# Performance work log

Measured on AMD Instinct MI355X. Metric: run time of the kernel, lower is better.

## Reference

```python
import jax, jax.numpy as jnp
import numpy as np
from jax.ops import segment_sum

N = 100000
E = 1600000
IN_DIM = 128
HID_DIM = 128
OUT_DIM = 64
BN_EPS = 1e-5


def setup_inputs() -> dict:
    key = jax.random.key(0)
    ks = jax.random.split(key, 8)
    h = jax.random.normal(ks[0], (N, IN_DIM), dtype=jnp.float32)
    src = jax.random.randint(ks[1], (E,), 0, N, dtype=jnp.int32)
    dst = jax.random.randint(ks[2], (E,), 0, N, dtype=jnp.int32)
    # GraphConv weights (glorot-ish scale)
    W1 = jax.random.normal(ks[3], (IN_DIM, HID_DIM), dtype=jnp.float32) / np.sqrt(IN_DIM)
    b1 = jnp.zeros((HID_DIM,), dtype=jnp.float32)
    W2 = jax.random.normal(ks[4], (HID_DIM, OUT_DIM), dtype=jnp.float32) / np.sqrt(HID_DIM)
    b2 = jnp.zeros((OUT_DIM,), dtype=jnp.float32)
    gamma = jnp.ones((HID_DIM,), dtype=jnp.float32)
    beta = jnp.zeros((HID_DIM,), dtype=jnp.float32)
    return {"h": h, "W1": W1, "b1": b1, "W2": W2, "b2": b2,
            "gamma": gamma, "beta": beta, "src": src, "dst": dst}


def _graph_conv(h, W, b, src, dst):
    # DGL GraphConv, norm='both':
    # out = D_dst^{-1/2} * A^T (D_src^{-1/2} * h) W + b, degrees clamped to >=1
    ones = jnp.ones((E,), dtype=h.dtype)
    deg_out = jnp.clip(segment_sum(ones, src, num_segments=N), 1.0)  # out-degree of src
    deg_in = jnp.clip(segment_sum(ones, dst, num_segments=N), 1.0)   # in-degree of dst
    h = h * jax.lax.rsqrt(deg_out)[:, None]
    # apply weight before aggregation when it reduces/keeps dim (DGL optimization)
    if W.shape[0] >= W.shape[1]:
        h = h @ W
        agg = segment_sum(h[src], dst, num_segments=N)  # [N, out_feat]
    else:
        agg = segment_sum(h[src], dst, num_segments=N) @ W
    return agg * jax.lax.rsqrt(deg_in)[:, None] + b


def reference(h, W1, b1, W2, b2, gamma, beta, src, dst):
    h = _graph_conv(h, W1, b1, src, dst)           # [N, HID_DIM]
    # BatchNorm1d, training mode: batch stats over node axis, biased variance
    mean = jnp.mean(h, axis=0)
    var = jnp.mean((h - mean) ** 2, axis=0)
    h = (h - mean) * jax.lax.rsqrt(var + BN_EPS) * gamma + beta
    h = jax.nn.relu(h)
    # dropout p=0.0 -> identity
    h = _graph_conv(h, W2, b2, src, dst)           # [N, OUT_DIM]
    return h
```

## Files before the change

### kernel.cpp

```cpp
#include <hip/hip_runtime.h>

#define NN 100000
#define NE 1600000
#define NB 391
#define CAP 5120
#define EPB 4096
#define BN_EPS 1e-5f

typedef _Float16 f16;
typedef _Float16 f16x4 __attribute__((ext_vector_type(4)));
typedef _Float16 f16x8 __attribute__((ext_vector_type(8)));
typedef float f32x4v __attribute__((ext_vector_type(4)));

__global__ __launch_bounds__(256) void kInit(const float* __restrict__ W1,
                                             const float* __restrict__ W2,
                                             f16* __restrict__ W1t,
                                             f16* __restrict__ W2t,
                                             int* __restrict__ curD,
                                             int* __restrict__ curS,
                                             float* __restrict__ stats) {
    int idx = blockIdx.x * 256 + threadIdx.x;
    if (idx < NB) { curD[idx] = idx * CAP; curS[idx] = idx * CAP; }
    if (idx < 512) stats[idx] = 0.f;
    if (idx < 16384) {
        int n = idx >> 7, k = idx & 127;
        W1t[idx] = (f16)W1[k * 128 + n];
    } else if (idx < 24576) {
        int j = idx - 16384;
        int n = j >> 7, k = j & 127;
        W2t[j] = (f16)W2[k * 64 + n];
    }
}

__global__ __launch_bounds__(256) void kC(const int* __restrict__ src,
                                          const int* __restrict__ dst,
                                          int* __restrict__ curD,
                                          int* __restrict__ curS,
                                          unsigned* __restrict__ pairs,
                                          unsigned char* __restrict__ srcBuck) {
    __shared__ int hD[NB], hS[NB], bD_[NB], bS_[NB];
    for (int i = threadIdx.x; i < NB; i += 256) { hD[i] = 0; hS[i] = 0; }
    __syncthreads();
    int e0 = blockIdx.x * EPB;
    int e1 = min(e0 + EPB, NE);
    for (int e = e0 + threadIdx.x; e < e1; e += 256) {
        atomicAdd(&hD[dst[e] >> 8], 1);
        atomicAdd(&hS[src[e] >> 8], 1);
    }
    __syncthreads();
    for (int i = threadIdx.x; i < NB; i += 256) {
        bD_[i] = hD[i] ? atomicAdd(&curD[i], hD[i]) : 0;
        bS_[i] = hS[i] ? atomicAdd(&curS[i], hS[i]) : 0;
        hD[i] = 0; hS[i] = 0;
    }
    __syncthreads();
    for (int e = e0 + threadIdx.x; e < e1; e += 256) {
        int d = dst[e], s = src[e];
        int db = d >> 8, sb = s >> 8;
        int rD = atomicAdd(&hD[db], 1);
        int posD = bD_[db] + rD;
        int limD = (db + 1) * CAP - 1;
        if (posD > limD) posD = limD;
        pairs[posD] = ((unsigned)s << 8) | (unsigned)(d & 255);
        int rS = atomicAdd(&hS[sb], 1);
        int posS = bS_[sb] + rS;
        int limS = (sb + 1) * CAP - 1;
        if (posS > limS) posS = limS;
        srcBuck[posS] = (unsigned char)(s & 255);
    }
}

__global__ __launch_bounds__(256) void kDE(const unsigned* __restrict__ pairs,
                                           const unsigned char* __restrict__ srcBuck,
                                           const int* __restrict__ curD,
                                           const int* __restrict__ curS,
                                           int* __restrict__ rowS,
                                           int* __restrict__ rowE,
                                           int* __restrict__ col,
                                           int* __restrict__ degO) {
    __shared__ int cnt[256], s[256];
    int t = threadIdx.x;
    if (blockIdx.x < NB) {
        int b = blockIdx.x;
        int p0 = b * CAP, p1 = curD[b];
        cnt[t] = 0;
        __syncthreads();
        for (int p = p0 + t; p < p1; p += 256)
            atomicAdd(&cnt[pairs[p] & 255u], 1);
        __syncthreads();
        int v = cnt[t];
        s[t] = v;
        __syncthreads();
        for (int off = 1; off < 256; off <<= 1) {
            int x = (t >= off) ? s[t - off] : 0;
            __syncthreads();
            s[t] += x;
            __syncthreads();
        }
        int excl = s[t] - v;
        int node = b * 256 + t;
        if (node < NN) { rowS[node] = p0 + excl; rowE[node] = p0 + excl + v; }
        cnt[t] = excl;
        __syncthreads();
        for (int p = p0 + t; p < p1; p += 256) {
            unsigned e = pairs[p];
            int r = atomicAdd(&cnt[e & 255u], 1);
            col[p0 + r] = (int)(e >> 8);
        }
    } else {
        int b = blockIdx.x - NB;
        int p0 = b * CAP, p1 = curS[b];
        cnt[t] = 0;
        __syncthreads();
        for (int p = p0 + t; p < p1; p += 256)
            atomicAdd(&cnt[srcBuck[p]], 1);
        __syncthreads();
        int node = b * 256 + t;
        if (node < NN) degO[node] = cnt[t];
    }
}

__global__ __launch_bounds__(256) void k_gemm1(const float* __restrict__ h,
                                               const f16* __restrict__ W1t,
                                               const int* __restrict__ degO,
                                               f16* __restrict__ x1h) {
    __shared__ f16 Ah[128 * 128];
    __shared__ f16 Bt[128 * 128];
    int tid = threadIdx.x;
    int row0 = blockIdx.x * 128;
#pragma unroll
    for (int p = 0; p < 8; ++p) {
        int fi = p * 256 + tid;
        int r = fi >> 4, c = fi & 15;
        uint4 v = *(const uint4*)&W1t[fi * 8];
        *(uint4*)&Bt[r * 128 + ((c ^ (r & 7)) * 8)] = v;
    }
#pragma unroll
    for (int p = 0; p < 16; ++p) {
        int fi = p * 256 + tid;
        int r = fi >> 5, c4 = fi & 31;
        int grow = row0 + r;
        float4 av = float4{0.f, 0.f, 0.f, 0.f};
        float dv = 1.f;
        if (grow < NN) {
            av = *(const float4*)&h[(size_t)grow * 128 + c4 * 4];
            dv = (float)degO[grow];
        }
        float rs = rsqrtf(fmaxf(dv, 1.f));
        f16x4 t;
        t[0] = (f16)(av.x * rs); t[1] = (f16)(av.y * rs);
        t[2] = (f16)(av.z * rs); t[3] = (f16)(av.w * rs);
        int c8 = c4 >> 1, off = (c4 & 1) * 4;
        *(f16x4*)&Ah[r * 128 + ((c8 ^ (r & 7)) * 8) + off] = t;
    }
    __syncthreads();
    int l = tid & 63, w = tid >> 6;
    int lr = l & 15, g = l >> 4;
    int m0 = w * 32;
    f16x8 a[2][4];
#pragma unroll
    for (int m = 0; m < 2; ++m)
#pragma unroll
        for (int kk = 0; kk < 4; ++kk) {
            int row = m0 + m * 16 + lr;
            a[m][kk] = *(f16x8*)&Ah[row * 128 + (((kk * 4 + g) ^ (row & 7)) * 8)];
        }
    f32x4v acc[2][8];
#pragma unroll
    for (int m = 0; m < 2; ++m)
#pragma unroll
        for (int n = 0; n < 8; ++n) acc[m][n] = f32x4v{0.f, 0.f, 0.f, 0.f};
#pragma unroll
    for (int n = 0; n < 8; ++n) {
        int colr = n * 16 + lr;
        f16x8 b[4];
#pragma unroll
        for (int kk = 0; kk < 4; ++kk)
            b[kk] = *(f16x8*)&Bt[colr * 128 + (((kk * 4 + g) ^ (colr & 7)) * 8)];
#pragma unroll
        for (int m = 0; m < 2; ++m)
#pragma unroll
            for (int kk = 0; kk < 4; ++kk)
                acc[m][n] = __builtin_amdgcn_mfma_f32_16x16x32_f16(a[m][kk], b[kk], acc[m][n], 0, 0, 0);
    }
    __syncthreads();
#pragma unroll
    for (int m = 0; m < 2; ++m)
#pragma unroll
        for (int n = 0; n < 8; ++n)
#pragma unroll
            for (int q = 0; q < 4; ++q) {
                int row = m0 + m * 16 + g * 4 + q;
                Ah[row * 128 + n * 16 + lr] = (f16)acc[m][n][q];
            }
    __syncthreads();
#pragma unroll
    for (int p = 0; p < 8; ++p) {
        int idx = p * 64 + l;
        int r = idx >> 4, c = idx & 15;
        int row = m0 + r, grow = row0 + row;
        uint4 v = *(uint4*)&Ah[row * 128 + c * 8];
        if (grow < NN) *(uint4*)&x1h[(size_t)grow * 128 + c * 8] = v;
    }
}

__global__ __launch_bounds__(256) void k_gather1(const f16* __restrict__ x1h,
                                                 const int* __restrict__ rowS,
                                                 const int* __restrict__ rowE,
                                                 const int* __restrict__ col,
                                                 const float* __restrict__ b1,
                                                 f16* __restrict__ y1h) {
    int node = blockIdx.x * 16 + (threadIdx.x >> 4);
    int f8 = threadIdx.x & 15;
    if (node >= NN) return;
    int s0 = rowS[node], s1 = rowE[node];
    const uint4* x4 = (const uint4*)x1h;
    float acc[8] = {0.f, 0.f, 0.f, 0.f, 0.f, 0.f, 0.f, 0.f};
    int j = s0;
    for (; j + 7 < s1; j += 8) {
        uint4 v[8];
#pragma unroll
        for (int u = 0; u < 8; ++u)
            v[u] = x4[(size_t)col[j + u] * 16 + f8];
#pragma unroll
        for (int u = 0; u < 8; ++u) {
            const f16* hp = (const f16*)&v[u];
#pragma unroll
            for (int k = 0; k < 8; ++k) acc[k] += (float)hp[k];
        }
    }
    for (; j + 3 < s1; j += 4) {
        uint4 v[4];
#pragma unroll
        for (int u = 0; u < 4; ++u)
            v[u] = x4[(size_t)col[j + u] * 16 + f8];
#pragma unroll
        for (int u = 0; u < 4; ++u) {
            const f16* hp = (const f16*)&v[u];
#pragma unroll
            for (int k = 0; k < 8; ++k) acc[k] += (float)hp[k];
        }
    }
    for (; j < s1; ++j) {
        uint4 v = x4[(size_t)col[j] * 16 + f8];
        const f16* hp = (const f16*)&v;
#pragma unroll
        for (int k = 0; k < 8; ++k) acc[k] += (float)hp[k];
    }
    float rs = rsqrtf(fmaxf((float)(s1 - s0), 1.f));
    const float4* b4 = (const float4*)b1;
    float4 ba = b4[f8 * 2], bb = b4[f8 * 2 + 1];
    f16x8 o;
    o[0] = (f16)(acc[0] * rs + ba.x); o[1] = (f16)(acc[1] * rs + ba.y);
    o[2] = (f16)(acc[2] * rs + ba.z); o[3] = (f16)(acc[3] * rs + ba.w);
    o[4] = (f16)(acc[4] * rs + bb.x); o[5] = (f16)(acc[5] * rs + bb.y);
    o[6] = (f16)(acc[6] * rs + bb.z); o[7] = (f16)(acc[7] * rs + bb.w);
    *(f16x8*)&y1h[(size_t)node * 128 + f8 * 8] = o;
}

__global__ __launch_bounds__(256) void k_bnstats(const f16* __restrict__ y1h,
                                                 float* __restrict__ stats) {
    int f = threadIdx.x & 127;
    int ro = threadIdx.x >> 7;
    float s = 0.f, ss = 0.f;
    for (int i = blockIdx.x * 2 + ro; i < NN; i += gridDim.x * 2) {
        float v = (float)y1h[(size_t)i * 128 + f];
        s += v;
        ss += v * v;
    }
    atomicAdd(&stats[f], s);
    atomicAdd(&stats[128 + f], ss);
}

__global__ __launch_bounds__(128) void k_bnfinal(float* __restrict__ stats,
                                                 const float* __restrict__ gamma,
                                                 const float* __restrict__ beta) {
    int f = threadIdx.x;
    float mean = stats[f] * (1.f / NN);
    float var = stats[128 + f] * (1.f / NN) - mean * mean;
    var = fmaxf(var, 0.f);
    float sc = gamma[f] * rsqrtf(var + BN_EPS);
    stats[256 + f] = sc;
    stats[384 + f] = beta[f] - mean * sc;
}

__global__ __launch_bounds__(256) void k_gemm2(const f16* __restrict__ y1h,
                                               const f16* __restrict__ W2t,
                                               const int* __restrict__ degO,
                                               const float* __restrict__ stats,
                                               f16* __restrict__ x2h) {
    __shared__ f16 Ah[128 * 128];
    __shared__ f16 Bt[64 * 128];
    __shared__ float sc[128], sh[128];
    int tid = threadIdx.x;
    int row0 = blockIdx.x * 128;
    if (tid < 128) { sc[tid] = stats[256 + tid]; sh[tid] = stats[384 + tid]; }
#pragma unroll
    for (int p = 0; p < 4; ++p) {
        int fi = p * 256 + tid;
        int r = fi >> 4, c = fi & 15;
        uint4 v = *(const uint4*)&W2t[fi * 8];
        *(uint4*)&Bt[r * 128 + ((c ^ (r & 7)) * 8)] = v;
    }
    __syncthreads();
#pragma unroll
    for (int p = 0; p < 8; ++p) {
        int fi = p * 256 + tid;
        int r = fi >> 4, c = fi & 15;
        int grow = row0 + r;
        f16x8 t;
        if (grow < NN) {
            uint4 v = *(const uint4*)&y1h[(size_t)grow * 128 + c * 8];
            const f16* hp = (const f16*)&v;
            float rs = rsqrtf(fmaxf((float)degO[grow], 1.f));
#pragma unroll
            for (int i = 0; i < 8; ++i) {
                int ch = c * 8 + i;
                float x = (float)hp[i] * sc[ch] + sh[ch];
                t[i] = (f16)(fmaxf(x, 0.f) * rs);
            }
        } else {
#pragma unroll
            for (int i = 0; i < 8; ++i) t[i] = (f16)0.f;
        }
        *(f16x8*)&Ah[r * 128 + ((c ^ (r & 7)) * 8)] = t;
    }
    __syncthreads();
    int l = tid & 63, w = tid >> 6;
    int lr = l & 15, g = l >> 4;
    int m0 = w * 32;
    f16x8 a[2][4];
#pragma unroll
    for (int m = 0; m < 2; ++m)
#pragma unroll
        for (int kk = 0; kk < 4; ++kk) {
            int row = m0 + m * 16 + lr;
            a[m][kk] = *(f16x8*)&Ah[row * 128 + (((kk * 4 + g) ^ (row & 7)) * 8)];
        }
    f32x4v acc[2][4];
#pragma unroll
    for (int m = 0; m < 2; ++m)
#pragma unroll
        for (int n = 0; n < 4; ++n) acc[m][n] = f32x4v{0.f, 0.f, 0.f, 0.f};
#pragma unroll
    for (int n = 0; n < 4; ++n) {
        int colr = n * 16 + lr;
        f16x8 b[4];
#pragma unroll
        for (int kk = 0; kk < 4; ++kk)
            b[kk] = *(f16x8*)&Bt[colr * 128 + (((kk * 4 + g) ^ (colr & 7)) * 8)];
#pragma unroll
        for (int m = 0; m < 2; ++m)
#pragma unroll
            for (int kk = 0; kk < 4; ++kk)
                acc[m][n] = __builtin_amdgcn_mfma_f32_16x16x32_f16(a[m][kk], b[kk], acc[m][n], 0, 0, 0);
    }
    __syncthreads();
#pragma unroll
    for (int m = 0; m < 2; ++m)
#pragma unroll
        for (int n = 0; n < 4; ++n)
#pragma unroll
            for (int q = 0; q < 4; ++q) {
                int row = m0 + m * 16 + g * 4 + q;
                Ah[row * 64 + n * 16 + lr] = (f16)acc[m][n][q];
            }
    __syncthreads();
#pragma unroll
    for (int p = 0; p < 4; ++p) {
        int idx = p * 64 + l;
        int r = idx >> 3, c = idx & 7;
        int row = m0 + r, grow = row0 + row;
        uint4 v = *(uint4*)&Ah[row * 64 + c * 8];
        if (grow < NN) *(uint4*)&x2h[(size_t)grow * 64 + c * 8] = v;
    }
}

__global__ __launch_bounds__(256) void k_gather2(const f16* __restrict__ x2h,
                                                 const int* __restrict__ rowS,
                                                 const int* __restrict__ rowE,
                                                 const int* __restrict__ col,
                                                 const float* __restrict__ b2,
                                                 float* __restrict__ out) {
    int node = blockIdx.x * 32 + (threadIdx.x >> 3);
    int f8 = threadIdx.x & 7;
    if (node >= NN) return;
    int s0 = rowS[node], s1 = rowE[node];
    const uint4* x4 = (const uint4*)x2h;
    float acc[8] = {0.f, 0.f, 0.f, 0.f, 0.f, 0.f, 0.f, 0.f};
    int j = s0;
    for (; j + 7 < s1; j += 8) {
        uint4 v[8];
#pragma unroll
        for (int u = 0; u < 8; ++u)
            v[u] = x4[(size_t)col[j + u] * 8 + f8];
#pragma unroll
        for (int u = 0; u < 8; ++u) {
            const f16* hp = (const f16*)&v[u];
#pragma unroll
            for (int k = 0; k < 8; ++k) acc[k] += (float)hp[k];
        }
    }
    for (; j + 3 < s1; j += 4) {
        uint4 v[4];
#pragma unroll
        for (int u = 0; u < 4; ++u)
            v[u] = x4[(size_t)col[j + u] * 8 + f8];
#pragma unroll
        for (int u = 0; u < 4; ++u) {
            const f16* hp = (const f16*)&v[u];
#pragma unroll
            for (int k = 0; k < 8; ++k) acc[k] += (float)hp[k];
        }
    }
    for (; j < s1; ++j) {
        uint4 v = x4[(size_t)col[j] * 8 + f8];
        const f16* hp = (const f16*)&v;
#pragma unroll
        for (int k = 0; k < 8; ++k) acc[k] += (float)hp[k];
    }
    float rs = rsqrtf(fmaxf((float)(s1 - s0), 1.f));
    const float4* b4 = (const float4*)b2;
    float4 ba = b4[f8 * 2], bb = b4[f8 * 2 + 1];
    float4 o0, o1;
    o0.x = acc[0] * rs + ba.x; o0.y = acc[1] * rs + ba.y;
    o0.z = acc[2] * rs + ba.z; o0.w = acc[3] * rs + ba.w;
    o1.x = acc[4] * rs + bb.x; o1.y = acc[5] * rs + bb.y;
    o1.z = acc[6] * rs + bb.z; o1.w = acc[7] * rs + bb.w;
    *(float4*)&out[(size_t)node * 64 + f8 * 8] = o0;
    *(float4*)&out[(size_t)node * 64 + f8 * 8 + 4] = o1;
}

extern "C" void kernel_launch(void* const* d_in, const int* in_sizes, int n_in,
                              void* d_out, int out_size, void* d_ws, size_t ws_size,
                              hipStream_t stream) {
    const float* h     = (const float*)d_in[0];
    const float* W1    = (const float*)d_in[1];
    const float* b1    = (const float*)d_in[2];
    const float* W2    = (const float*)d_in[3];
    const float* b2    = (const float*)d_in[4];
    const float* gamma = (const float*)d_in[5];
    const float* beta  = (const float*)d_in[6];
    const int*   src   = (const int*)d_in[7];
    const int*   dst   = (const int*)d_in[8];
    float* out = (float*)d_out;

    const size_t BSZ = (size_t)NB * CAP;

    int* base = (int*)d_ws;
    float* stats = (float*)base;
    int* curD = base + 512;
    int* curS = curD + NB;
    int* rowS = curS + NB;
    int* rowE = rowS + NN;
    int* degO = rowE + NN;
    int* col  = degO + NN;
    unsigned* pairs = (unsigned*)(col + BSZ);
    unsigned char* srcBuck = (unsigned char*)(pairs + BSZ);
    size_t o = (size_t)(col + BSZ - base) + BSZ + (BSZ + 3) / 4;
    o = (o + 3) & ~(size_t)3;
    f16* W1t = (f16*)(base + o);
    f16* W2t = W1t + 16384;
    o += 8192 + 4096;
    f16* x1h = (f16*)(base + o);
    o += (size_t)NN * 64;
    f16* y1h = (f16*)(base + o);
    f16* x2h = x1h;

    kInit<<<97, 256, 0, stream>>>(W1, W2, W1t, W2t, curD, curS, stats);

    int bgrid = (NE + EPB - 1) / EPB;
    kC<<<bgrid, 256, 0, stream>>>(src, dst, curD, curS, pairs, srcBuck);
    kDE<<<2 * NB, 256, 0, stream>>>(pairs, srcBuck, curD, curS, rowS, rowE, col, degO);

    int ggrid = (NN + 127) / 128;
    k_gemm1<<<ggrid, 256, 0, stream>>>(h, W1t, degO, x1h);
    k_gather1<<<(NN + 15) / 16, 256, 0, stream>>>(x1h, rowS, rowE, col, b1, y1h);
    k_bnstats<<<512, 256, 0, stream>>>(y1h, stats);
    k_bnfinal<<<1, 128, 0, stream>>>(stats, gamma, beta);
    k_gemm2<<<ggrid, 256, 0, stream>>>(y1h, W2t, degO, stats, x2h);
    k_gather2<<<(NN + 31) / 32, 256, 0, stream>>>(x2h, rowS, rowE, col, b2, out);
}
```

Baseline: 275.4 us.

## Fuse BN stats into gather1, stage edges in LDS, two-pass CSR sort

Several changes at once. BatchNorm sum and sum-of-squares are now computed inside the first gather kernel via wave shuffles and per-block partials, followed by a small reduction kernel. This removes the separate pass that re-read y1h. The edge-bucketing kernel caches src/dst in shared memory instead of reading them twice. The CSR build stages each bucket in LDS and does a coarse radix pass before the per-node scatter, which should make writes to col more local. The GEMMs compute the degree normalisation once per row in shared memory. The gather loops drop the 8-way unrolled path, which may reduce memory-level parallelism.

```diff
diff --git a/kernel.cpp b/kernel.cpp
--- a/kernel.cpp
+++ b/kernel.cpp
@@ -5,6 +5,7 @@
 #define NB 391
 #define CAP 5120
 #define EPB 4096
+#define NG1 6250
 #define BN_EPS 1e-5f
 
 typedef _Float16 f16;
@@ -38,24 +39,28 @@
                                           int* __restrict__ curS,
                                           unsigned* __restrict__ pairs,
                                           unsigned char* __restrict__ srcBuck) {
+    __shared__ int sA[EPB], dA[EPB];
     __shared__ int hD[NB], hS[NB], bD_[NB], bS_[NB];
-    for (int i = threadIdx.x; i < NB; i += 256) { hD[i] = 0; hS[i] = 0; }
+    int t = threadIdx.x;
+    for (int i = t; i < NB; i += 256) { hD[i] = 0; hS[i] = 0; }
     __syncthreads();
     int e0 = blockIdx.x * EPB;
-    int e1 = min(e0 + EPB, NE);
-    for (int e = e0 + threadIdx.x; e < e1; e += 256) {
-        atomicAdd(&hD[dst[e] >> 8], 1);
-        atomicAdd(&hS[src[e] >> 8], 1);
-    }
-    __syncthreads();
-    for (int i = threadIdx.x; i < NB; i += 256) {
+    int ne = min(EPB, NE - e0);
+    for (int i = t; i < ne; i += 256) {
+        int s = src[e0 + i], d = dst[e0 + i];
+        sA[i] = s; dA[i] = d;
+        atomicAdd(&hD[d >> 8], 1);
+        atomicAdd(&hS[s >> 8], 1);
+    }
+    __syncthreads();
+    for (int i = t; i < NB; i += 256) {
         bD_[i] = hD[i] ? atomicAdd(&curD[i], hD[i]) : 0;
         bS_[i] = hS[i] ? atomicAdd(&curS[i], hS[i]) : 0;
         hD[i] = 0; hS[i] = 0;
     }
     __syncthreads();
-    for (int e = e0 + threadIdx.x; e < e1; e += 256) {
-        int d = dst[e], s = src[e];
+    for (int i = t; i < ne; i += 256) {
+        int s = sA[i], d = dA[i];
         int db = d >> 8, sb = s >> 8;
         int rD = atomicAdd(&hD[db], 1);
         int posD = bD_[db] + rD;
@@ -78,40 +83,56 @@
                                            int* __restrict__ rowE,
                                            int* __restrict__ col,
                                            int* __restrict__ degO) {
-    __shared__ int cnt[256], s[256];
+    __shared__ unsigned bufA[CAP], bufB[CAP];
+    __shared__ int binC[256], binS[256];
+    __shared__ int cnt[256], csc[256];
     int t = threadIdx.x;
     if (blockIdx.x < NB) {
         int b = blockIdx.x;
-        int p0 = b * CAP, p1 = curD[b];
-        cnt[t] = 0;
-        __syncthreads();
-        for (int p = p0 + t; p < p1; p += 256)
-            atomicAdd(&cnt[pairs[p] & 255u], 1);
-        __syncthreads();
-        int v = cnt[t];
-        s[t] = v;
+        int p0 = b * CAP;
+        int n = min(curD[b] - p0, CAP);
+        binC[t] = 0; cnt[t] = 0;
+        __syncthreads();
+        for (int i = t; i < n; i += 256) {
+            unsigned v = pairs[p0 + i];
+            bufA[i] = v;
+            atomicAdd(&binC[v >> 17], 1);
+            atomicAdd(&cnt[v & 255u], 1);
+        }
+        __syncthreads();
+        int vB = binC[t], vN = cnt[t];
+        binS[t] = vB; csc[t] = vN;
         __syncthreads();
         for (int off = 1; off < 256; off <<= 1) {
-            int x = (t >= off) ? s[t - off] : 0;
+            int xB = (t >= off) ? binS[t - off] : 0;
+            int xN = (t >= off) ? csc[t - off] : 0;
             __syncthreads();
-            s[t] += x;
+            binS[t] += xB; csc[t] += xN;
             __syncthreads();
         }
-        int excl = s[t] - v;
         int node = b * 256 + t;
-        if (node < NN) { rowS[node] = p0 + excl; rowE[node] = p0 + excl + v; }
-        cnt[t] = excl;
-        __syncthreads();
-        for (int p = p0 + t; p < p1; p += 256) {
-            unsigned e = pairs[p];
-            int r = atomicAdd(&cnt[e & 255u], 1);
-            col[p0 + r] = (int)(e >> 8);
+        int nodeStart = csc[t] - vN;
+        if (node < NN) { rowS[node] = p0 + nodeStart; rowE[node] = p0 + nodeStart + vN; }
+        binC[t] = binS[t] - vB;
+        cnt[t] = nodeStart;
+        __syncthreads();
+        for (int i = t; i < n; i += 256) {
+            unsigned v = bufA[i];
+            int pos = atomicAdd(&binC[v >> 17], 1);
+            bufB[pos] = v;
+        }
+        __syncthreads();
+        for (int i = t; i < n; i += 256) {
+            unsigned v = bufB[i];
+            int r = atomicAdd(&cnt[v & 255u], 1);
+            col[p0 + r] = (int)(v >> 8);
         }
     } else {
         int b = blockIdx.x - NB;
-        int p0 = b * CAP, p1 = curS[b];
         cnt[t] = 0;
         __syncthreads();
+        int p0 = b * CAP;
+        int p1 = min(curS[b], p0 + CAP);
         for (int p = p0 + t; p < p1; p += 256)
             atomicAdd(&cnt[srcBuck[p]], 1);
         __syncthreads();
@@ -126,8 +147,14 @@
                                                f16* __restrict__ x1h) {
     __shared__ f16 Ah[128 * 128];
     __shared__ f16 Bt[128 * 128];
+    __shared__ float rsA[128];
     int tid = threadIdx.x;
     int row0 = blockIdx.x * 128;
+    if (tid < 128) {
+        int r = row0 + tid;
+        float d = (r < NN) ? (float)degO[r] : 1.f;
+        rsA[tid] = rsqrtf(fmaxf(d, 1.f));
+    }
 #pragma unroll
     for (int p = 0; p < 8; ++p) {
         int fi = p * 256 + tid;
@@ -135,18 +162,15 @@
         uint4 v = *(const uint4*)&W1t[fi * 8];
         *(uint4*)&Bt[r * 128 + ((c ^ (r & 7)) * 8)] = v;
     }
+    __syncthreads();
 #pragma unroll
     for (int p = 0; p < 16; ++p) {
         int fi = p * 256 + tid;
         int r = fi >> 5, c4 = fi & 31;
         int grow = row0 + r;
         float4 av = float4{0.f, 0.f, 0.f, 0.f};
-        float dv = 1.f;
-        if (grow < NN) {
-            av = *(const float4*)&h[(size_t)grow * 128 + c4 * 4];
-            dv = (float)degO[grow];
-        }
-        float rs = rsqrtf(fmaxf(dv, 1.f));
+        if (grow < NN) av = *(const float4*)&h[(size_t)grow * 128 + c4 * 4];
+        float rs = rsA[r];
         f16x4 t;
         t[0] = (f16)(av.x * rs); t[1] = (f16)(av.y * rs);
         t[2] = (f16)(av.z * rs); t[3] = (f16)(av.w * rs);
@@ -209,40 +233,32 @@
                                                  const int* __restrict__ rowE,
                                                  const int* __restrict__ col,
                                                  const float* __restrict__ b1,
-                                                 f16* __restrict__ y1h) {
-    int node = blockIdx.x * 16 + (threadIdx.x >> 4);
-    int f8 = threadIdx.x & 15;
-    if (node >= NN) return;
+                                                 f16* __restrict__ y1h,
+                                                 float* __restrict__ part) {
+    __shared__ float red[4 * 16 * 16];
+    int tid = threadIdx.x;
+    int bid = blockIdx.x;
+    int node = bid * 16 + (tid >> 4);
+    int f8 = tid & 15;
     int s0 = rowS[node], s1 = rowE[node];
     const uint4* x4 = (const uint4*)x1h;
     float acc[8] = {0.f, 0.f, 0.f, 0.f, 0.f, 0.f, 0.f, 0.f};
     int j = s0;
-    for (; j + 7 < s1; j += 8) {
-        uint4 v[8];
-#pragma unroll
-        for (int u = 0; u < 8; ++u)
-            v[u] = x4[(size_t)col[j + u] * 16 + f8];
-#pragma unroll
-        for (int u = 0; u < 8; ++u) {
-            const f16* hp = (const f16*)&v[u];
-#pragma unroll
-            for (int k = 0; k < 8; ++k) acc[k] += (float)hp[k];
-        }
-    }
     for (; j + 3 < s1; j += 4) {
-        uint4 v[4];
-#pragma unroll
-        for (int u = 0; u < 4; ++u)
-            v[u] = x4[(size_t)col[j + u] * 16 + f8];
-#pragma unroll
-        for (int u = 0; u < 4; ++u) {
-            const f16* hp = (const f16*)&v[u];
-#pragma unroll
-            for (int k = 0; k < 8; ++k) acc[k] += (float)hp[k];
-        }
+        int a0 = col[j], a1 = col[j + 1], a2 = col[j + 2], a3 = col[j + 3];
+        uint4 v0 = x4[(size_t)a0 * 16 + f8];
+        uint4 v1 = x4[(size_t)a1 * 16 + f8];
+        uint4 v2 = x4[(size_t)a2 * 16 + f8];
+        uint4 v3 = x4[(size_t)a3 * 16 + f8];
+        const f16* h0 = (const f16*)&v0; const f16* h1 = (const f16*)&v1;
+        const f16* h2 = (const f16*)&v2; const f16* h3 = (const f16*)&v3;
+#pragma unroll
+        for (int k = 0; k < 8; ++k)
+            acc[k] += (float)h0[k] + (float)h1[k] + (float)h2[k] + (float)h3[k];
     }
     for (; j < s1; ++j) {
-        uint4 v = x4[(size_t)col[j] * 16 + f8];
+        int a = col[j];
+        uint4 v = x4[(size_t)a * 16 + f8];
         const f16* hp = (const f16*)&v;
 #pragma unroll
         for (int k = 0; k < 8; ++k) acc[k] += (float)hp[k];
@@ -256,20 +272,40 @@
     o[4] = (f16)(acc[4] * rs + bb.x); o[5] = (f16)(acc[5] * rs + bb.y);
     o[6] = (f16)(acc[6] * rs + bb.z); o[7] = (f16)(acc[7] * rs + bb.w);
     *(f16x8*)&y1h[(size_t)node * 128 + f8 * 8] = o;
-}
-
-__global__ __launch_bounds__(256) void k_bnstats(const f16* __restrict__ y1h,
-                                                 float* __restrict__ stats) {
-    int f = threadIdx.x & 127;
-    int ro = threadIdx.x >> 7;
-    float s = 0.f, ss = 0.f;
-    for (int i = blockIdx.x * 2 + ro; i < NN; i += gridDim.x * 2) {
-        float v = (float)y1h[(size_t)i * 128 + f];
-        s += v;
-        ss += v * v;
-    }
-    atomicAdd(&stats[f], s);
-    atomicAdd(&stats[128 + f], ss);
+    float sv[8], qv[8];
+#pragma unroll
+    for (int k = 0; k < 8; ++k) { sv[k] = (float)o[k]; qv[k] = sv[k] * sv[k]; }
+#pragma unroll
+    for (int mask = 16; mask <= 32; mask <<= 1) {
+#pragma unroll
+        for (int k = 0; k < 8; ++k) {
+            sv[k] += __shfl_xor(sv[k], mask);
+            qv[k] += __shfl_xor(qv[k], mask);
+        }
+    }
+    int w = tid >> 6, lane = tid & 63;
+    if (lane < 16) {
+#pragma unroll
+        for (int k = 0; k < 8; ++k) {
+            red[w * 256 + lane * 16 + k] = sv[k];
+            red[w * 256 + lane * 16 + 8 + k] = qv[k];
+        }
+    }
+    __syncthreads();
+    int f8_ = tid & 15, idx = tid >> 4;
+    float tot = red[0 * 256 + f8_ * 16 + idx] + red[1 * 256 + f8_ * 16 + idx]
+              + red[2 * 256 + f8_ * 16 + idx] + red[3 * 256 + f8_ * 16 + idx];
+    int slot = (idx < 8) ? (f8_ * 8 + idx) : (128 + f8_ * 8 + (idx - 8));
+    part[(size_t)bid * 256 + slot] = tot;
+}
+
+__global__ __launch_bounds__(256) void k_bnred(const float* __restrict__ part,
+                                               float* __restrict__ stats) {
+    int t = threadIdx.x;
+    float loc = 0.f;
+    for (int b = blockIdx.x; b < NG1; b += gridDim.x)
+        loc += part[(size_t)b * 256 + t];
+    atomicAdd(&stats[t], loc);
 }
 
 __global__ __launch_bounds__(128) void k_bnfinal(float* __restrict__ stats,
@@ -291,10 +327,16 @@
                                                f16* __restrict__ x2h) {
     __shared__ f16 Ah[128 * 128];
     __shared__ f16 Bt[64 * 128];
-    __shared__ float sc[128], sh[128];
+    __shared__ float sc[128], sh[128], rsA[128];
     int tid = threadIdx.x;
     int row0 = blockIdx.x * 128;
-    if (tid < 128) { sc[tid] = stats[256 + tid]; sh[tid] = stats[384 + tid]; }
+    if (tid < 128) {
+        sc[tid] = stats[256 + tid];
+        sh[tid] = stats[384 + tid];
+        int r = row0 + tid;
+        float d = (r < NN) ? (float)degO[r] : 1.f;
+        rsA[tid] = rsqrtf(fmaxf(d, 1.f));
+    }
 #pragma unroll
     for (int p = 0; p < 4; ++p) {
         int fi = p * 256 + tid;
@@ -312,7 +354,7 @@
         if (grow < NN) {
             uint4 v = *(const uint4*)&y1h[(size_t)grow * 128 + c * 8];
             const f16* hp = (const f16*)&v;
-            float rs = rsqrtf(fmaxf((float)degO[grow], 1.f));
+            float rs = rsA[r];
 #pragma unroll
             for (int i = 0; i < 8; ++i) {
                 int ch = c * 8 + i;
@@ -389,18 +431,6 @@
     const uint4* x4 = (const uint4*)x2h;
     float acc[8] = {0.f, 0.f, 0.f, 0.f, 0.f, 0.f, 0.f, 0.f};
     int j = s0;
-    for (; j + 7 < s1; j += 8) {
-        uint4 v[8];
-#pragma unroll
-        for (int u = 0; u < 8; ++u)
-            v[u] = x4[(size_t)col[j + u] * 8 + f8];
-#pragma unroll
-        for (int u = 0; u < 8; ++u) {
-            const f16* hp = (const f16*)&v[u];
-#pragma unroll
-            for (int k = 0; k < 8; ++k) acc[k] += (float)hp[k];
-        }
-    }
     for (; j + 3 < s1; j += 4) {
         uint4 v[4];
 #pragma unroll
@@ -457,7 +487,8 @@
     int* col  = degO + NN;
     unsigned* pairs = (unsigned*)(col + BSZ);
     unsigned char* srcBuck = (unsigned char*)(pairs + BSZ);
-    size_t o = (size_t)(col + BSZ - base) + BSZ + (BSZ + 3) / 4;
+    float* part = (float*)(pairs + BSZ + (BSZ + 3) / 4);
+    size_t o = (size_t)(col + BSZ - base) + BSZ + (BSZ + 3) / 4 + (size_t)NG1 * 256;
     o = (o + 3) & ~(size_t)3;
     f16* W1t = (f16*)(base + o);
     f16* W2t = W1t + 16384;
@@ -475,8 +506,8 @@
 
     int ggrid = (NN + 127) / 128;
     k_gemm1<<<ggrid, 256, 0, stream>>>(h, W1t, degO, x1h);
-    k_gather1<<<(NN + 15) / 16, 256, 0, stream>>>(x1h, rowS, rowE, col, b1, y1h);
-    k_bnstats<<<512, 256, 0, stream>>>(y1h, stats);
+    k_gather1<<<NG1, 256, 0, stream>>>(x1h, rowS, rowE, col, b1, y1h, part);
+    k_bnred<<<64, 256, 0, stream>>>(part, stats);
     k_bnfinal<<<1, 128, 0, stream>>>(stats, gamma, beta);
     k_gemm2<<<ggrid, 256, 0, stream>>>(y1h, W2t, degO, stats, x2h);
     k_gather2<<<(NN + 31) / 32, 256, 0, stream>>>(x2h, rowS, rowE, col, b2, out);
```

Result: faster. 253.3 us (-8.0%).
